# Kernel tuning notes

Hardware: AMD Instinct MI355X
Metric: run time of the kernel (lower is better)

Reference implementation:

```python
import jax, jax.numpy as jnp
import numpy as np

MA_K = 2 * 125 + 1  # 251, moving-average kernel
MV_K = 4 * 125 + 1  # 501, moving-variance kernel
EPS = 1e-5


def _avg_pool1d(x, K):
    """PyTorch F.avg_pool1d(stride=1, padding=(K-1)//2, count_include_pad=True)
    computed in O(L) via prefix sums. x: (B, C, L) -> (B, C, L)."""
    pad = (K - 1) // 2
    xp = jnp.pad(x, ((0, 0), (0, 0), (pad, pad)))  # zero pad, length L+K-1
    c = jnp.pad(jnp.cumsum(xp, axis=-1), ((0, 0), (0, 0), (1, 0)))  # length L+K
    return (c[..., K:] - c[..., :-K]) / K  # divide by K always (count_include_pad)


def setup_inputs() -> dict:
    key = jax.random.key(0)
    x = jax.random.normal(key, (8192, 1, 3750), dtype=jnp.float32)
    return {"x": x}


def reference(x):
    # global z-norm per (batch, channel); torch.std is unbiased (ddof=1)
    x = (x - jnp.mean(x, axis=2, keepdims=True)) / (
        jnp.std(x, axis=2, keepdims=True, ddof=1) + EPS)
    # remove moving average (kernel 251)
    x = x - _avg_pool1d(x, MA_K)
    # rescale by moving std (kernel 501)
    x = x / (jnp.sqrt(_avg_pool1d(x * x, MV_K)) + EPS)
    return x
```

## Files before the change

### kernel.cpp

```cpp
#include <hip/hip_runtime.h>
#include <math.h>

namespace {

constexpr int L      = 3750;
constexpr int NPAIR  = L / 2;
constexpr int BLK    = 256;
constexpr int CH     = 15;
constexpr int NCHUNK = L / CH;
constexpr float EPS  = 1e-5f;

__device__ __forceinline__ float frcp(float x)  { return __builtin_amdgcn_rcpf(x); }
__device__ __forceinline__ float fsqrt(float x) { return __builtin_amdgcn_sqrtf(x); }

__global__ __launch_bounds__(BLK)
void preproc_kernel(const float* __restrict__ in, float* __restrict__ out) {
    __shared__ float sy[L];
    __shared__ float sp[L + 1];
    __shared__ float sred[8];

    const int tid  = threadIdx.x;
    const int lane = tid & 63;
    const int wave = tid >> 6;
    const size_t rowoff = (size_t)blockIdx.x * (size_t)L;
    const float* rin  = in  + rowoff;
    float*       rout = out + rowoff;

    {
        const float2* rin2 = reinterpret_cast<const float2*>(rin);
        float2* sy2 = reinterpret_cast<float2*>(sy);
        for (int i = tid; i < NPAIR; i += BLK) sy2[i] = rin2[i];
    }
    __syncthreads();

    float mean, zinv;
    {
        float loc[CH];
        float cy = 0.f, cy2 = 0.f;
        if (tid < NCHUNK) {
            const int base = tid * CH;
            #pragma unroll
            for (int j = 0; j < CH; ++j) {
                loc[j] = cy;
                const float v = sy[base + j];
                cy  += v;
                cy2 += v * v;
            }
        }
        float iy  = (tid < NCHUNK) ? cy  : 0.f;
        float iy2 = (tid < NCHUNK) ? cy2 : 0.f;
        const float vy = iy;
        #pragma unroll
        for (int d = 1; d < 64; d <<= 1) {
            const float u  = __shfl_up(iy,  (unsigned)d, 64);
            const float u2 = __shfl_up(iy2, (unsigned)d, 64);
            if (lane >= d) { iy += u; iy2 += u2; }
        }
        if (lane == 63) { sred[wave] = iy; sred[4 + wave] = iy2; }
        __syncthreads();
        float woff = 0.f;
        for (int w = 0; w < wave; ++w) woff += sred[w];
        const float totY  = sred[0] + sred[1] + sred[2] + sred[3];
        const float totY2 = sred[4] + sred[5] + sred[6] + sred[7];
        mean = totY * (1.f / (float)L);
        const float var = (totY2 - totY * mean) * (1.f / (float)(L - 1));
        zinv = frcp(fsqrt(var) + EPS);
        const float excl = woff + iy - vy;
        if (tid < NCHUNK) {
            const int base = tid * CH;
            #pragma unroll
            for (int j = 0; j < CH; ++j) sp[base + j] = excl + loc[j];
            if (tid == NCHUNK - 1) sp[L] = excl + cy;
        }
        __syncthreads();
    }

    {
        const float zinv251 = zinv * (1.f / 251.f);
        float loc[CH];
        float ct = 0.f;
        if (tid < NCHUNK) {
            const int base = tid * CH;
            #pragma unroll
            for (int j = 0; j < CH; ++j) {
                const int i  = base + j;
                const int lo = (i > 125) ? (i - 125) : 0;
                const int hi = (i + 126 < L) ? (i + 126) : L;
                const float winY = sp[hi] - sp[lo] - (float)(hi - lo) * mean;
                const float z    = (sy[i] - mean) * zinv;
                const float t    = z - winY * zinv251;
                sy[i]  = t;
                loc[j] = ct;
                ct += t * t;
            }
        }
        const float vt = (tid < NCHUNK) ? ct : 0.f;
        float it = vt;
        #pragma unroll
        for (int d = 1; d < 64; d <<= 1) {
            const float u = __shfl_up(it, (unsigned)d, 64);
            if (lane >= d) it += u;
        }
        if (lane == 63) sred[wave] = it;
        __syncthreads();
        float woff = 0.f;
        for (int w = 0; w < wave; ++w) woff += sred[w];
        const float excl = woff + it - vt;
        if (tid < NCHUNK) {
            const int base = tid * CH;
            #pragma unroll
            for (int j = 0; j < CH; ++j) sp[base + j] = excl + loc[j];
            if (tid == NCHUNK - 1) sp[L] = excl + ct;
        }
        __syncthreads();
    }

    {
        const float inv501 = 1.f / 501.f;
        const float2* st2 = reinterpret_cast<const float2*>(sy);
        for (int i = tid; i < NPAIR; i += BLK) {
            const int i0 = 2 * i;
            const float2 tv = st2[i];
            float2 r;
            {
                const int lo = (i0 > 250) ? (i0 - 250) : 0;
                const int hi = (i0 + 251 < L) ? (i0 + 251) : L;
                float mv = (sp[hi] - sp[lo]) * inv501;
                mv = fmaxf(mv, 0.f);
                r.x = tv.x * frcp(fsqrt(mv) + EPS);
            }
            {
                const int i1 = i0 + 1;
                const int lo = (i1 > 250) ? (i1 - 250) : 0;
                const int hi = (i1 + 251 < L) ? (i1 + 251) : L;
                float mv = (sp[hi] - sp[lo]) * inv501;
                mv = fmaxf(mv, 0.f);
                r.y = tv.y * frcp(fsqrt(mv) + EPS);
            }
            reinterpret_cast<float2*>(rout)[i] = r;
        }
    }
}

}

extern "C" void kernel_launch(void* const* d_in, const int* in_sizes, int n_in,
                              void* d_out, int out_size, void* d_ws, size_t ws_size,
                              hipStream_t stream) {
    const float* x = (const float*)d_in[0];
    float* out = (float*)d_out;
    const int rows = in_sizes[0] / L;
    preproc_kernel<<<rows, BLK, 0, stream>>>(x, out);
}
```

Measured before the change: 54.27 us.

## Keep row values in registers and drop second LDS array to raise occupancy

Removes the separate shared buffer for the row by keeping each thread's 15 samples in registers, reusing the prefix-sum array for input staging and for output staging. Shared memory per block roughly halves, and launch bounds now request 8 blocks per SIMD-level occupancy, aiming for more resident blocks to hide latency. The trade-off is extra register pressure plus two more barriers and an extra LDS round trip to coalesce the final store.

```diff
diff --git a/kernel.cpp b/kernel.cpp
--- a/kernel.cpp
+++ b/kernel.cpp
@@ -13,10 +13,9 @@
 __device__ __forceinline__ float frcp(float x)  { return __builtin_amdgcn_rcpf(x); }
 __device__ __forceinline__ float fsqrt(float x) { return __builtin_amdgcn_sqrtf(x); }
 
-__global__ __launch_bounds__(BLK)
+__global__ __launch_bounds__(BLK, 8)
 void preproc_kernel(const float* __restrict__ in, float* __restrict__ out) {
-    __shared__ float sy[L];
-    __shared__ float sp[L + 1];
+    __shared__ __align__(16) float sp[L + 1];
     __shared__ float sred[8];
 
     const int tid  = threadIdx.x;
@@ -28,117 +27,113 @@
 
     {
         const float2* rin2 = reinterpret_cast<const float2*>(rin);
-        float2* sy2 = reinterpret_cast<float2*>(sy);
-        for (int i = tid; i < NPAIR; i += BLK) sy2[i] = rin2[i];
+        float2* sp2 = reinterpret_cast<float2*>(sp);
+        for (int i = tid; i < NPAIR; i += BLK) sp2[i] = rin2[i];
     }
     __syncthreads();
 
-    float mean, zinv;
-    {
-        float loc[CH];
-        float cy = 0.f, cy2 = 0.f;
-        if (tid < NCHUNK) {
-            const int base = tid * CH;
-            #pragma unroll
-            for (int j = 0; j < CH; ++j) {
-                loc[j] = cy;
-                const float v = sy[base + j];
-                cy  += v;
-                cy2 += v * v;
-            }
+    float y[CH];
+    float cy = 0.f, cy2 = 0.f;
+    const int base = tid * CH;
+    if (tid < NCHUNK) {
+        #pragma unroll
+        for (int j = 0; j < CH; ++j) {
+            const float v = sp[base + j];
+            y[j] = v;
+            cy  += v;
+            cy2 += v * v;
         }
-        float iy  = (tid < NCHUNK) ? cy  : 0.f;
-        float iy2 = (tid < NCHUNK) ? cy2 : 0.f;
-        const float vy = iy;
-        #pragma unroll
-        for (int d = 1; d < 64; d <<= 1) {
-            const float u  = __shfl_up(iy,  (unsigned)d, 64);
-            const float u2 = __shfl_up(iy2, (unsigned)d, 64);
-            if (lane >= d) { iy += u; iy2 += u2; }
-        }
-        if (lane == 63) { sred[wave] = iy; sred[4 + wave] = iy2; }
-        __syncthreads();
-        float woff = 0.f;
-        for (int w = 0; w < wave; ++w) woff += sred[w];
-        const float totY  = sred[0] + sred[1] + sred[2] + sred[3];
-        const float totY2 = sred[4] + sred[5] + sred[6] + sred[7];
-        mean = totY * (1.f / (float)L);
-        const float var = (totY2 - totY * mean) * (1.f / (float)(L - 1));
-        zinv = frcp(fsqrt(var) + EPS);
-        const float excl = woff + iy - vy;
-        if (tid < NCHUNK) {
-            const int base = tid * CH;
-            #pragma unroll
-            for (int j = 0; j < CH; ++j) sp[base + j] = excl + loc[j];
-            if (tid == NCHUNK - 1) sp[L] = excl + cy;
-        }
-        __syncthreads();
     }
+    float iy = cy, iy2 = cy2;
+    #pragma unroll
+    for (int d = 1; d < 64; d <<= 1) {
+        const float u  = __shfl_up(iy,  (unsigned)d, 64);
+        const float u2 = __shfl_up(iy2, (unsigned)d, 64);
+        if (lane >= d) { iy += u; iy2 += u2; }
+    }
+    if (lane == 63) { sred[wave] = iy; sred[4 + wave] = iy2; }
+    __syncthreads();
+    float woff = 0.f;
+    for (int w = 0; w < wave; ++w) woff += sred[w];
+    const float totY  = sred[0] + sred[1] + sred[2] + sred[3];
+    const float totY2 = sred[4] + sred[5] + sred[6] + sred[7];
+    const float mean  = totY * (1.f / (float)L);
+    const float var   = (totY2 - totY * mean) * (1.f / (float)(L - 1));
+    const float zinv  = frcp(fsqrt(var) + EPS);
 
     {
+        float run = woff + iy - cy;
+        if (tid < NCHUNK) {
+            #pragma unroll
+            for (int j = 0; j < CH; ++j) { sp[base + j] = run; run += y[j]; }
+            if (tid == NCHUNK - 1) sp[L] = run;
+        }
+    }
+    __syncthreads();
+
+    float ct = 0.f;
+    {
         const float zinv251 = zinv * (1.f / 251.f);
-        float loc[CH];
-        float ct = 0.f;
         if (tid < NCHUNK) {
-            const int base = tid * CH;
             #pragma unroll
             for (int j = 0; j < CH; ++j) {
                 const int i  = base + j;
                 const int lo = (i > 125) ? (i - 125) : 0;
                 const int hi = (i + 126 < L) ? (i + 126) : L;
                 const float winY = sp[hi] - sp[lo] - (float)(hi - lo) * mean;
-                const float z    = (sy[i] - mean) * zinv;
+                const float z    = (y[j] - mean) * zinv;
                 const float t    = z - winY * zinv251;
-                sy[i]  = t;
-                loc[j] = ct;
-                ct += t * t;
+                y[j] = t;
+                ct  += t * t;
             }
         }
-        const float vt = (tid < NCHUNK) ? ct : 0.f;
-        float it = vt;
-        #pragma unroll
-        for (int d = 1; d < 64; d <<= 1) {
-            const float u = __shfl_up(it, (unsigned)d, 64);
-            if (lane >= d) it += u;
+    }
+    float it = ct;
+    #pragma unroll
+    for (int d = 1; d < 64; d <<= 1) {
+        const float u = __shfl_up(it, (unsigned)d, 64);
+        if (lane >= d) it += u;
+    }
+    if (lane == 63) sred[wave] = it;
+    __syncthreads();
+    float woff2 = 0.f;
+    for (int w = 0; w < wave; ++w) woff2 += sred[w];
+
+    {
+        float run = woff2 + it - ct;
+        if (tid < NCHUNK) {
+            #pragma unroll
+            for (int j = 0; j < CH; ++j) { sp[base + j] = run; run += y[j] * y[j]; }
+            if (tid == NCHUNK - 1) sp[L] = run;
         }
-        if (lane == 63) sred[wave] = it;
-        __syncthreads();
-        float woff = 0.f;
-        for (int w = 0; w < wave; ++w) woff += sred[w];
-        const float excl = woff + it - vt;
-        if (tid < NCHUNK) {
-            const int base = tid * CH;
-            #pragma unroll
-            for (int j = 0; j < CH; ++j) sp[base + j] = excl + loc[j];
-            if (tid == NCHUNK - 1) sp[L] = excl + ct;
-        }
-        __syncthreads();
     }
+    __syncthreads();
 
     {
         const float inv501 = 1.f / 501.f;
-        const float2* st2 = reinterpret_cast<const float2*>(sy);
-        for (int i = tid; i < NPAIR; i += BLK) {
-            const int i0 = 2 * i;
-            const float2 tv = st2[i];
-            float2 r;
-            {
-                const int lo = (i0 > 250) ? (i0 - 250) : 0;
-                const int hi = (i0 + 251 < L) ? (i0 + 251) : L;
+        if (tid < NCHUNK) {
+            #pragma unroll
+            for (int j = 0; j < CH; ++j) {
+                const int i  = base + j;
+                const int lo = (i > 250) ? (i - 250) : 0;
+                const int hi = (i + 251 < L) ? (i + 251) : L;
                 float mv = (sp[hi] - sp[lo]) * inv501;
                 mv = fmaxf(mv, 0.f);
-                r.x = tv.x * frcp(fsqrt(mv) + EPS);
+                y[j] = y[j] * frcp(fsqrt(mv) + EPS);
             }
-            {
-                const int i1 = i0 + 1;
-                const int lo = (i1 > 250) ? (i1 - 250) : 0;
-                const int hi = (i1 + 251 < L) ? (i1 + 251) : L;
-                float mv = (sp[hi] - sp[lo]) * inv501;
-                mv = fmaxf(mv, 0.f);
-                r.y = tv.y * frcp(fsqrt(mv) + EPS);
-            }
-            reinterpret_cast<float2*>(rout)[i] = r;
         }
+    }
+    __syncthreads();
+
+    if (tid < NCHUNK) {
+        #pragma unroll
+        for (int j = 0; j < CH; ++j) sp[base + j] = y[j];
+    }
+    __syncthreads();
+    {
+        const float2* sp2 = reinterpret_cast<const float2*>(sp);
+        float2* rout2 = reinterpret_cast<float2*>(rout);
+        for (int i = tid; i < NPAIR; i += BLK) rout2[i] = sp2[i];
     }
 }
 
```

Result: faster. 52.75 us (-2.8%).
